# Optimization experiments

Measured on AMD Instinct MI355X. Metric: run time of the kernel, lower is better.

The kernel has to match this reference:

```python
import jax, jax.numpy as jnp
import numpy as np

B, S, H = 16, 4096, 1152
GRID = 64  # 64x64 patch grid -> S = GRID*GRID
OUT_LEN = 256  # pooled soft tokens (k = sqrt(S/OUT_LEN) = 4)


def setup_inputs() -> dict:
    key = jax.random.key(0)
    x = jax.random.normal(key, (B, S, H), dtype=jnp.float32)
    i = jnp.arange(S)
    # position_ids[..., 0] = x coord, [..., 1] = y coord on the patch grid
    pos = jnp.stack([i % GRID, i // GRID], axis=-1).astype(jnp.int32)  # [S, 2]
    position_ids = jnp.broadcast_to(pos, (B, S, 2))
    return {"x": x, "position_ids": position_ids, "output_length": OUT_LEN}


def reference(x, position_ids, output_length):
    b, s, h = x.shape
    # zero out padding positions (pos == [-1, -1])
    padding = jnp.all(position_ids == -1, axis=-1)  # [B, S]
    x = jnp.where(padding[..., None], jnp.float32(0.0), x)

    k = int((s // output_length) ** 0.5)
    k2 = k * k

    pos = jnp.maximum(position_ids, 0)
    max_x = jnp.max(pos[..., 0], axis=-1, keepdims=True) + 1  # [B, 1]
    # bucket index of each patch: (x//k) + (max_x//k) * (y//k)
    kidx = pos[..., 0] // k + (max_x // k) * pos[..., 1] // 1 * 0 + (pos[..., 0] // k) * 0 + (pos[..., 0] // k)
    kidx = pos[..., 0] // k + (max_x // k) * (pos[..., 1] // k)  # [B, S]

    # scatter-mean: segment_sum over flattened (batch-offset) bucket ids, / k^2
    seg = (kidx + jnp.arange(b)[:, None] * output_length).reshape(-1)
    pooled = jax.ops.segment_sum(
        x.reshape(b * s, h), seg, num_segments=b * output_length
    ).reshape(b, output_length, h) / jnp.float32(k2)

    root_hidden = jnp.float32(h ** 0.5)
    return pooled * root_hidden
```

## Files before the change

### kernel.cpp

```cpp
#include <hip/hip_runtime.h>


#define BB 16
#define SS 4096
#define HH 1152
#define OUTL 256
#define KK 4
#define K2 16
#define H4 (HH / 4)
#define HP (H4 / 2)
#define BPB 144
#define NB 3

__global__ __launch_bounds__(256) void pool_fused(const float* __restrict__ x,
                                                  const int* __restrict__ pos,
                                                  float* __restrict__ out) {
    int blk = blockIdx.x;
    int b = blk / BPB;
    int bl = blk - b * BPB;
    int t = threadIdx.x;
    int lidx = bl * 256 + t;
    int bo_local = lidx / HP;
    int c = lidx - bo_local * HP;
    int lo = (bl * 256) / HP;

    const int2* p2 = reinterpret_cast<const int2*>(pos) + (size_t)b * SS;

    int2 rr[SS / 256];
#pragma unroll
    for (int i = 0; i < SS / 256; ++i) rr[i] = p2[t + i * 256];

    int m = 0;
#pragma unroll
    for (int i = 0; i < SS / 256; ++i) m = max(m, rr[i].x);
#pragma unroll
    for (int o = 32; o > 0; o >>= 1) m = max(m, __shfl_down(m, o));

    __shared__ int wred[4];
    __shared__ int lrows[NB * K2];
    if ((t & 63) == 0) wred[t >> 6] = m;
    if (t < NB * K2) lrows[t] = -1;
    __syncthreads();
    int mxk = (max(max(wred[0], wred[1]), max(wred[2], wred[3])) + 1) / KK;

#pragma unroll
    for (int i = 0; i < SS / 256; ++i) {
        int2 xy = rr[i];
        if (xy.x == -1 && xy.y == -1) continue;
        int px = max(xy.x, 0), py = max(xy.y, 0);
        int kidx = px / KK + mxk * (py / KK);
        unsigned rel = (unsigned)(kidx - lo);
        if (rel < NB) lrows[rel * K2 + (py & (KK - 1)) * KK + (px & (KK - 1))] = t + i * 256;
    }
    __syncthreads();

    int rel = bo_local - lo;
    int ridx[K2];
#pragma unroll
    for (int j = 0; j < K2; ++j) ridx[j] = lrows[rel * K2 + j];

    const float4* xb = reinterpret_cast<const float4*>(x) + (size_t)b * SS * H4 + c;
    float4 a0 = {0.f, 0.f, 0.f, 0.f};
    float4 a1 = {0.f, 0.f, 0.f, 0.f};
#pragma unroll
    for (int j = 0; j < K2; ++j) {
        int row = ridx[j];
        if (row >= 0) {
            const float4* p = xb + (size_t)row * H4;
            float4 v0 = p[0], v1 = p[HP];
            a0.x += v0.x; a0.y += v0.y; a0.z += v0.z; a0.w += v0.w;
            a1.x += v1.x; a1.y += v1.y; a1.z += v1.z; a1.w += v1.w;
        }
    }
    const float scale = 2.1213203435596424f;
    a0.x *= scale; a0.y *= scale; a0.z *= scale; a0.w *= scale;
    a1.x *= scale; a1.y *= scale; a1.z *= scale; a1.w *= scale;

    int bo = b * OUTL + bo_local;
    float4* ob = reinterpret_cast<float4*>(out) + (size_t)bo * H4 + c;
    ob[0] = a0;
    ob[HP] = a1;
}

extern "C" void kernel_launch(void* const* d_in, const int* in_sizes, int n_in,
                              void* d_out, int out_size, void* d_ws, size_t ws_size,
                              hipStream_t stream) {
    const float* x = (const float*)d_in[0];
    const int* pos = (const int*)d_in[1];
    float* out = (float*)d_out;

    pool_fused<<<BB * BPB, 256, 0, stream>>>(x, pos, out);
}
```

Baseline: 60.94 us.

## Process three chunks per block to amortize position scan, use branchless weighted loads

Each block now handles three 256-thread chunks (768 float4 pairs) instead of one, so the per-block read of all 4096 position pairs and the bucket table build are shared across three times as much output work. The grid shrinks from 2304 to 768 blocks, with a launch-bounds occupancy hint added. The gather loop becomes branchless: padding rows are clamped to row 0 and multiplied by a zero weight, so all 16 loads can issue unconditionally. The tradeoffs are fewer blocks to hide latency and extra loads of row 0 wherever padding occurs.

Result: no change. 61.29 us (+0.6%).

```diff
diff --git a/kernel.cpp b/kernel.cpp
--- a/kernel.cpp
+++ b/kernel.cpp
@@ -9,20 +9,18 @@
 #define K2 16
 #define H4 (HH / 4)
 #define HP (H4 / 2)
-#define BPB 144
-#define NB 3
+#define GPB 48
+#define NB 7
 
-__global__ __launch_bounds__(256) void pool_fused(const float* __restrict__ x,
-                                                  const int* __restrict__ pos,
-                                                  float* __restrict__ out) {
+__global__ __launch_bounds__(256, 3) void pool_fused(const float* __restrict__ x,
+                                                     const int* __restrict__ pos,
+                                                     float* __restrict__ out) {
     int blk = blockIdx.x;
-    int b = blk / BPB;
-    int bl = blk - b * BPB;
+    int b = blk / GPB;
+    int g = blk - b * GPB;
     int t = threadIdx.x;
-    int lidx = bl * 256 + t;
-    int bo_local = lidx / HP;
-    int c = lidx - bo_local * HP;
-    int lo = (bl * 256) / HP;
+    int base = g * 768;
+    int lo = base / HP;
 
     const int2* p2 = reinterpret_cast<const int2*>(pos) + (size_t)b * SS;
 
@@ -54,32 +52,46 @@
     }
     __syncthreads();
 
-    int rel = bo_local - lo;
-    int ridx[K2];
+    const float scale = 2.1213203435596424f;
+    const float4* xbase = reinterpret_cast<const float4*>(x) + (size_t)b * SS * H4;
+    float4* obase = reinterpret_cast<float4*>(out) + (size_t)b * OUTL * H4;
+
 #pragma unroll
-    for (int j = 0; j < K2; ++j) ridx[j] = lrows[rel * K2 + j];
+    for (int it = 0; it < 3; ++it) {
+        int lidx = base + it * 256 + t;
+        int bo_local = lidx / HP;
+        int c = lidx - bo_local * HP;
+        int rel = bo_local - lo;
 
-    const float4* xb = reinterpret_cast<const float4*>(x) + (size_t)b * SS * H4 + c;
-    float4 a0 = {0.f, 0.f, 0.f, 0.f};
-    float4 a1 = {0.f, 0.f, 0.f, 0.f};
+        int ridx[K2];
+        float w[K2];
 #pragma unroll
-    for (int j = 0; j < K2; ++j) {
-        int row = ridx[j];
-        if (row >= 0) {
-            const float4* p = xb + (size_t)row * H4;
+        for (int j = 0; j < K2; ++j) {
+            int row = lrows[rel * K2 + j];
+            w[j] = (row >= 0) ? 1.0f : 0.0f;
+            ridx[j] = max(row, 0);
+        }
+
+        const float4* xb = xbase + c;
+        float4 a0 = {0.f, 0.f, 0.f, 0.f};
+        float4 a1 = {0.f, 0.f, 0.f, 0.f};
+#pragma unroll
+        for (int j = 0; j < K2; ++j) {
+            const float4* p = xb + (size_t)ridx[j] * H4;
             float4 v0 = p[0], v1 = p[HP];
-            a0.x += v0.x; a0.y += v0.y; a0.z += v0.z; a0.w += v0.w;
-            a1.x += v1.x; a1.y += v1.y; a1.z += v1.z; a1.w += v1.w;
+            float wj = w[j];
+            a0.x = fmaf(v0.x, wj, a0.x); a0.y = fmaf(v0.y, wj, a0.y);
+            a0.z = fmaf(v0.z, wj, a0.z); a0.w = fmaf(v0.w, wj, a0.w);
+            a1.x = fmaf(v1.x, wj, a1.x); a1.y = fmaf(v1.y, wj, a1.y);
+            a1.z = fmaf(v1.z, wj, a1.z); a1.w = fmaf(v1.w, wj, a1.w);
         }
+        a0.x *= scale; a0.y *= scale; a0.z *= scale; a0.w *= scale;
+        a1.x *= scale; a1.y *= scale; a1.z *= scale; a1.w *= scale;
+
+        float4* ob = obase + (size_t)bo_local * H4 + c;
+        ob[0] = a0;
+        ob[HP] = a1;
     }
-    const float scale = 2.1213203435596424f;
-    a0.x *= scale; a0.y *= scale; a0.z *= scale; a0.w *= scale;
-    a1.x *= scale; a1.y *= scale; a1.z *= scale; a1.w *= scale;
-
-    int bo = b * OUTL + bo_local;
-    float4* ob = reinterpret_cast<float4*>(out) + (size_t)bo * H4 + c;
-    ob[0] = a0;
-    ob[HP] = a1;
 }
 
 extern "C" void kernel_launch(void* const* d_in, const int* in_sizes, int n_in,
@@ -89,5 +101,5 @@
     const int* pos = (const int*)d_in[1];
     float* out = (float*)d_out;
 
-    pool_fused<<<BB * BPB, 256, 0, stream>>>(x, pos, out);
+    pool_fused<<<BB * GPB, 256, 0, stream>>>(x, pos, out);
 }
```
